# Kernel tuning notes

Measured on AMD Instinct MI355X. Metric: run time of the kernel, lower is better.

The kernel has to match this reference:

```python
import jax, jax.numpy as jnp
import numpy as np

B, T, E, H, R = 4, 256, 128, 8, 64
D = E // H


def _xavier(k, fan_in, fan_out, gain=1.0):
    a = gain * np.sqrt(6.0 / (fan_in + fan_out))
    return jax.random.uniform(k, (fan_in, fan_out), minval=-a, maxval=a, dtype=jnp.float32)


def setup_inputs() -> dict:
    key = jax.random.key(0)
    ks = jax.random.split(key, 16)
    g = 1.0 / np.sqrt(2.0)  # gain used for q/k/v when qkv_same_dim
    return {
        "query": jax.random.normal(ks[0], (B, T, E), jnp.float32),
        "velocity": jax.random.normal(ks[1], (B, T, 3, E), jnp.float32),
        "edge_feature": jax.random.normal(ks[2], (B, T, T, R), jnp.float32),
        "edge_direction": jax.random.normal(ks[3], (B, T, T, 3), jnp.float32),
        "cutoff": jax.random.uniform(ks[4], (B, T, T), jnp.float32),
        "Wq": _xavier(ks[5], E, E, g), "bq": jnp.zeros((E,), jnp.float32),
        "Wk": _xavier(ks[6], E, E, g), "bk": jnp.zeros((E,), jnp.float32),
        "Wv": _xavier(ks[7], E, 3 * E, g), "bv": jnp.zeros((3 * E,), jnp.float32),
        "Wo": _xavier(ks[8], E, 3 * E), "bo": jnp.zeros((3 * E,), jnp.float32),
        "Wvel": _xavier(ks[9], E, 3 * E), "bvel": jnp.zeros((3 * E,), jnp.float32),
        "Wdk": _xavier(ks[10], R, E), "bdk": jnp.zeros((E,), jnp.float32),
        "Wdv": _xavier(ks[11], R, 3 * E), "bdv": jnp.zeros((3 * E,), jnp.float32),
    }


def reference(query, velocity, edge_feature, edge_direction, cutoff,
              Wq, bq, Wk, bk, Wv, bv, Wo, bo, Wvel, bvel, Wdk, bdk, Wdv, bdv):
    b, t, e = query.shape
    h = H
    d = e // h
    scaling = d ** -0.5
    # projections
    q = ((query @ Wq + bq) * scaling).reshape(b, t, 1, h, d)   # [b,t,1,h,d]
    k = (query @ Wk + bk).reshape(b, 1, t, h, d)                # [b,1,t,h,d]
    v = (query @ Wv + bv).reshape(b, 1, t, h, 3 * d)            # [b,1,t,h,3d]
    # RBF distance gates (dense pairwise)
    dk = jax.nn.silu(edge_feature @ Wdk + bdk).reshape(b, t, t, h, d)
    dv = jax.nn.silu(edge_feature @ Wdv + bdv).reshape(b, t, t, h, 3 * d)
    v = v * dv                                                  # [b,t,t,h,3d]
    v, vp1, vp2 = jnp.split(v, 3, axis=-1)                      # each [b,t,t,h,d]
    # velocity channel
    velp = velocity @ Wvel + bvel                               # [b,t,3,3e]
    w1, w2, w3 = jnp.split(velp, 3, axis=-1)                    # each [b,t,3,e]
    velocity_dot = (w1 * w2).sum(axis=2)                        # [b,t,e]
    vel_r = velocity.reshape(b, t, 3, h, d)
    # elementwise (non-dot-product) attention weights
    aw = q * k * dk / np.float32(np.sqrt(d))                    # [b,t,t,h,d]
    awf = jnp.nan_to_num(jax.nn.softmax(aw, axis=2))
    c = cutoff[..., None, None]                                 # [b,t,t,1,1]
    attn = (awf * c * v * (c != 0)).sum(axis=2).reshape(b, t, e)
    o1, o2, o3 = jnp.split(attn @ Wo + bo, 3, axis=-1)          # each [b,t,e]
    # equivariant vector path
    vec1 = vel_r[:, None] * vp1[:, :, :, None]                  # [b,t,t,3,h,d]
    vec2 = vp2[:, :, :, None] * edge_direction[..., None, None]
    vec = ((vec1 + vec2).reshape(b, t, t, 3, e) * (c != 0)).sum(axis=2)  # [b,t,3,e]
    dx = velocity_dot * o2 + o3                                 # [b,t,e]
    dvec = w3 * o1[:, :, None, :] + vec                         # [b,t,3,e]
    return dx, dvec
```

## Files before the change

kernel.cpp:

```cpp
#include <hip/hip_runtime.h>
#include <hip/hip_bf16.h>
#include <math.h>

#define TT 256
#define EE 128
#define TJ 16

typedef __attribute__((ext_vector_type(8))) short short8v;
typedef __attribute__((ext_vector_type(4))) float f32x4;

__device__ __forceinline__ float silu_f(float x) {
    return x * __builtin_amdgcn_rcpf(1.0f + __expf(-x));
}

__device__ __forceinline__ unsigned short f2bf(float f) {
    union { float f; unsigned u; } x; x.f = f;
    unsigned r = (x.u + 0x7FFFu + ((x.u >> 16) & 1u)) >> 16;
    return (unsigned short)r;
}

__device__ __forceinline__ unsigned cvt_pk_bf16(float lo, float hi) {
    unsigned r;
    asm("v_cvt_pk_bf16_f32 %0, %1, %2" : "=v"(r) : "v"(lo), "v"(hi));
    return r;
}

__device__ __forceinline__ float bflo(unsigned u) { return __uint_as_float(u << 16); }
__device__ __forceinline__ float bfhi(unsigned u) { return __uint_as_float(u & 0xffff0000u); }

__global__ __launch_bounds__(256) void packW_kernel(
    const float* __restrict__ Wdk, const float* __restrict__ Wdv,
    unsigned short* __restrict__ wfrag) {
    const int idx = blockIdx.x * 256 + threadIdx.x;
    const int lane = idx & 63;
    const int kh = (idx >> 6) & 1;
    const int nn = (idx >> 7) & 7;
    const int w = idx >> 10;
    const float* Wsel; int wstride, colbase;
    if (w == 0) { Wsel = Wdk; wstride = 128; colbase = 0; }
    else { Wsel = Wdv; wstride = 384; colbase = (w - 1) * 128; }
    const int lrow = lane >> 4;
    const int lcol = lane & 15;
    const int col = colbase + nn * 16 + lcol;
    unsigned short* dst = wfrag + (size_t)idx * 8;
#pragma unroll
    for (int e = 0; e < 8; ++e) {
        const int k = kh * 32 + lrow * 8 + e;
        dst[e] = f2bf(Wsel[k * wstride + col]);
    }
}

__global__ __launch_bounds__(256) void phaseA_kernel(
    const float* __restrict__ query, const float* __restrict__ velocity,
    const float* __restrict__ Wq, const float* __restrict__ bq,
    const float* __restrict__ Wk, const float* __restrict__ bk,
    const float* __restrict__ Wv, const float* __restrict__ bv,
    const float* __restrict__ Wvel, const float* __restrict__ bvel,
    float* __restrict__ qs_ws, float* __restrict__ kk_ws,
    float* __restrict__ vproj_ws, float* __restrict__ veldot_ws,
    float* __restrict__ w3_ws) {
    const int row = blockIdx.x;
    const int t = threadIdx.x;
    __shared__ float sIn[EE];
    __shared__ float sVel[3 * EE];
    __shared__ float sVelp[3 * 384];
    if (t < EE) sIn[t] = query[(size_t)row * EE + t];
    for (int idx = t; idx < 3 * EE; idx += 256)
        sVel[idx] = velocity[(size_t)row * 3 * EE + idx];
    __syncthreads();

    for (int o = t; o < 640; o += 256) {
        if (o < 128) {
            int c = o;
            float acc = bq[c];
#pragma unroll 8
            for (int r = 0; r < 128; ++r) acc = fmaf(sIn[r], Wq[r * 128 + c], acc);
            qs_ws[(size_t)row * 128 + c] = acc * 0.25f;
        } else if (o < 256) {
            int c = o - 128;
            float acc = bk[c];
#pragma unroll 8
            for (int r = 0; r < 128; ++r) acc = fmaf(sIn[r], Wk[r * 128 + c], acc);
            kk_ws[(size_t)row * 128 + c] = acc;
        } else {
            int c = o - 256;
            float acc = bv[c];
#pragma unroll 8
            for (int r = 0; r < 128; ++r) acc = fmaf(sIn[r], Wv[r * 384 + c], acc);
            vproj_ws[(size_t)row * 384 + c] = acc;
        }
    }
    for (int c = t; c < 384; c += 256) {
        float a0 = bvel[c], a1 = a0, a2 = a0;
#pragma unroll 8
        for (int r = 0; r < 128; ++r) {
            float w = Wvel[r * 384 + c];
            a0 = fmaf(sVel[r], w, a0);
            a1 = fmaf(sVel[128 + r], w, a1);
            a2 = fmaf(sVel[256 + r], w, a2);
        }
        sVelp[0 * 384 + c] = a0;
        sVelp[1 * 384 + c] = a1;
        sVelp[2 * 384 + c] = a2;
    }
    __syncthreads();
    if (t < 128) {
        int c = t;
        float vd = 0.f;
#pragma unroll
        for (int s = 0; s < 3; ++s)
            vd += sVelp[s * 384 + c] * sVelp[s * 384 + 128 + c];
        veldot_ws[(size_t)row * 128 + c] = vd;
#pragma unroll
        for (int s = 0; s < 3; ++s)
            w3_ws[((size_t)row * 3 + s) * 128 + c] = sVelp[s * 384 + 256 + c];
    }
}

__global__ __launch_bounds__(256, 4) void phaseB_kernel(
    const float* __restrict__ edge_feature, const float* __restrict__ edge_direction,
    const float* __restrict__ cutoff, const float* __restrict__ velocity,
    const unsigned short* __restrict__ wfrag,
    const float* __restrict__ bdk, const float* __restrict__ bdv,
    const float* __restrict__ qs_ws, const float* __restrict__ kk_ws,
    const float* __restrict__ vproj_ws,
    float* __restrict__ attn_ws, float* __restrict__ vec_ws) {
    const int blk = blockIdx.x;
    const int x = blk & 7;
    const int slot = blk >> 3;
    const int b = x >> 1;
    const int i = ((x & 1) << 7) + slot;
    const int row = b * TT + i;

    const int t = threadIdx.x;
    const int wave = t >> 6;
    const int lane = t & 63;
    const int lrow = lane >> 4;
    const int lcol = lane & 15;

    __shared__ __align__(16) unsigned char sEFb[16 * 128];
    __shared__ unsigned short sKD[128 * 18];
    __shared__ unsigned short sGV[3 * 128 * 18];
    __shared__ float sCut[TJ];
    __shared__ float sDirS[TJ * 3];
    __shared__ float sMrg[128][5];

    const float* Bsel;
    int colbase;
    if (wave == 0) { Bsel = bdk; colbase = 0; }
    else { Bsel = bdv; colbase = (wave - 1) * 128; }

    float biasv[8];
#pragma unroll
    for (int n = 0; n < 8; ++n)
        biasv[n] = Bsel[colbase + n * 16 + lcol];

    const unsigned short* wfbase = wfrag + ((size_t)wave * 1024 + lane) * 8;

    const float* gsrc = (wave == 0) ? (kk_ws + (size_t)(b * TT) * 128)
                                    : (vproj_ws + (size_t)(b * TT) * 384);
    const int gstride = (wave == 0) ? 128 : 384;

    const int grp = t >> 7;
    const int c = t & 127;
    const float qsc = qs_ws[(size_t)row * 128 + c] * 0.25f;

    float l = 0.f, A = 0.f;
    float v0 = 0.f, v1 = 0.f, v2 = 0.f;

    const size_t ef_base = (size_t)row * TT * 64;
    const size_t cut_base = (size_t)row * TT;
    const size_t dir_base = (size_t)row * TT * 3;
    const float* velbase = velocity + (size_t)(b * TT) * 384 + c;

    f32x4 pEf = ((const f32x4*)(edge_feature + ef_base))[t];
    float pCut = (t < TJ) ? cutoff[cut_base + t] : 0.f;
    float pDir = (t < TJ * 3) ? edge_direction[dir_base + t] : 0.f;

    for (int j0 = 0; j0 < TT; j0 += TJ) {
        {
            const int erow = t >> 4;
            const int kq = t & 15;
            unsigned plo = cvt_pk_bf16(pEf[0], pEf[1]);
            unsigned phi = cvt_pk_bf16(pEf[2], pEf[3]);
            const int byteoff = (kq * 8) ^ ((erow & 7) << 4);
            *(int2*)(sEFb + erow * 128 + byteoff) = make_int2((int)plo, (int)phi);
            if (t < TJ) sCut[t] = pCut;
            if (t < TJ * 3) sDirS[t] = pDir;
        }
        __syncthreads();

        {
            const int arow = lcol;
            const int swzb = (arow & 7) << 4;
            const short8v a0 = *(const short8v*)(sEFb + arow * 128 + ((lrow * 16) ^ swzb));
            const short8v a1 = *(const short8v*)(sEFb + arow * 128 + ((64 + lrow * 16) ^ swzb));
            const int jb = j0 + lrow * 4;

            float gg[8][4];
#pragma unroll
            for (int n = 0; n < 8; ++n) {
                const float* gp = gsrc + (size_t)jb * gstride + colbase + n * 16 + lcol;
                gg[n][0] = gp[0];
                gg[n][1] = gp[gstride];
                gg[n][2] = gp[2 * gstride];
                gg[n][3] = gp[3 * gstride];
            }
#pragma unroll
            for (int n = 0; n < 8; ++n) {
                const int col = colbase + n * 16 + lcol;
                const short8v b0 = *(const short8v*)(wfbase + (size_t)n * 1024);
                const short8v b1 = *(const short8v*)(wfbase + (size_t)n * 1024 + 512);
                f32x4 acc = {biasv[n], biasv[n], biasv[n], biasv[n]};
                acc = __builtin_amdgcn_mfma_f32_16x16x32_bf16(a0, b0, acc, 0, 0, 0);
                acc = __builtin_amdgcn_mfma_f32_16x16x32_bf16(a1, b1, acc, 0, 0, 0);
                const float r0 = gg[n][0] * silu_f(acc[0]);
                const float r1 = gg[n][1] * silu_f(acc[1]);
                const float r2 = gg[n][2] * silu_f(acc[2]);
                const float r3 = gg[n][3] * silu_f(acc[3]);
                const unsigned w01 = cvt_pk_bf16(r0, r1);
                const unsigned w23 = cvt_pk_bf16(r2, r3);
                unsigned short* dst;
                if (wave == 0) {
                    dst = &sKD[col * 18 + lrow * 4];
                } else {
                    const int plane = (col >> 4) % 3;
                    const int cch = (col / 48) * 16 + lcol;
                    dst = &sGV[plane * 2304 + cch * 18 + lrow * 4];
                }
                *(unsigned*)(dst) = w01;
                *(unsigned*)(dst + 2) = w23;
            }
        }

        {
            const int jn = (j0 + TJ) & 255;
            pEf = ((const f32x4*)(edge_feature + ef_base + (size_t)jn * 64))[t];
            pCut = (t < TJ) ? cutoff[cut_base + jn + t] : 0.f;
            pDir = (t < TJ * 3) ? edge_direction[dir_base + (size_t)jn * 3 + t] : 0.f;
        }
        __syncthreads();

        {
            const int jlo = grp * (TJ / 2);
#pragma unroll
            for (int q = 0; q < 4; ++q) {
                const int jj = jlo + 2 * q;
                const unsigned kd2 = *(const unsigned*)(&sKD[c * 18 + jj]);
                const unsigned vg2 = *(const unsigned*)(&sGV[0 * 2304 + c * 18 + jj]);
                const unsigned p12 = *(const unsigned*)(&sGV[1 * 2304 + c * 18 + jj]);
                const unsigned p22 = *(const unsigned*)(&sGV[2 * 2304 + c * 18 + jj]);
                const float cut0 = sCut[jj];
                const float cut1 = sCut[jj + 1];
                const float p0 = __expf(qsc * bflo(kd2));
                const float p1 = __expf(qsc * bfhi(kd2));
                l += p0 + p1;
                A = fmaf(p0 * cut0, bflo(vg2), A);
                A = fmaf(p1 * cut1, bfhi(vg2), A);
                if (cut0 != 0.0f) {
                    const float* vp = velbase + (size_t)(j0 + jj) * 384;
                    const float w1 = bflo(p12), w2 = bflo(p22);
                    v0 = fmaf(vp[0],   w1, fmaf(w2, sDirS[jj * 3 + 0], v0));
                    v1 = fmaf(vp[128], w1, fmaf(w2, sDirS[jj * 3 + 1], v1));
                    v2 = fmaf(vp[256], w1, fmaf(w2, sDirS[jj * 3 + 2], v2));
                }
                if (cut1 != 0.0f) {
                    const float* vp = velbase + (size_t)(j0 + jj + 1) * 384;
                    const float w1 = bfhi(p12), w2 = bfhi(p22);
                    v0 = fmaf(vp[0],   w1, fmaf(w2, sDirS[jj * 3 + 3], v0));
                    v1 = fmaf(vp[128], w1, fmaf(w2, sDirS[jj * 3 + 4], v1));
                    v2 = fmaf(vp[256], w1, fmaf(w2, sDirS[jj * 3 + 5], v2));
                }
            }
        }
        __syncthreads();
    }

    if (grp == 1) {
        sMrg[c][0] = l;  sMrg[c][1] = A;
        sMrg[c][2] = v0; sMrg[c][3] = v1; sMrg[c][4] = v2;
    }
    __syncthreads();
    if (grp == 0) {
        const float L = l + sMrg[c][0];
        const float Aa = A + sMrg[c][1];
        const float attn = (L > 0.f) ? (Aa * __builtin_amdgcn_rcpf(L)) : 0.f;
        attn_ws[(size_t)row * 128 + c] = attn;
        vec_ws[((size_t)row * 3 + 0) * 128 + c] = v0 + sMrg[c][2];
        vec_ws[((size_t)row * 3 + 1) * 128 + c] = v1 + sMrg[c][3];
        vec_ws[((size_t)row * 3 + 2) * 128 + c] = v2 + sMrg[c][4];
    }
}

__global__ __launch_bounds__(256) void phaseC_kernel(
    const float* __restrict__ Wo, const float* __restrict__ bo,
    const float* __restrict__ attn_ws, const float* __restrict__ veldot_ws,
    const float* __restrict__ w3_ws, const float* __restrict__ vec_ws,
    float* __restrict__ out) {
    const int row = blockIdx.x;
    const int t = threadIdx.x;
    __shared__ float sAttn[128];
    __shared__ float sO[384];
    if (t < 128) sAttn[t] = attn_ws[(size_t)row * 128 + t];
    __syncthreads();
    for (int o = t; o < 384; o += 256) {
        float acc = bo[o];
#pragma unroll 8
        for (int r = 0; r < 128; ++r) acc = fmaf(sAttn[r], Wo[r * 384 + o], acc);
        sO[o] = acc;
    }
    __syncthreads();
    if (t < 128) {
        int c = t;
        float o1 = sO[c], o2 = sO[128 + c], o3 = sO[256 + c];
        float dx = fmaf(veldot_ws[(size_t)row * 128 + c], o2, o3);
        out[(size_t)row * 128 + c] = dx;
#pragma unroll
        for (int s = 0; s < 3; ++s) {
            size_t idx = ((size_t)row * 3 + s) * 128 + c;
            out[131072 + idx] = fmaf(w3_ws[idx], o1, vec_ws[idx]);
        }
    }
}

extern "C" void kernel_launch(void* const* d_in, const int* in_sizes, int n_in,
                              void* d_out, int out_size, void* d_ws, size_t ws_size,
                              hipStream_t stream) {
    (void)in_sizes; (void)n_in; (void)out_size; (void)ws_size;
    const float* query          = (const float*)d_in[0];
    const float* velocity       = (const float*)d_in[1];
    const float* edge_feature   = (const float*)d_in[2];
    const float* edge_direction = (const float*)d_in[3];
    const float* cutoff         = (const float*)d_in[4];
    const float* Wq   = (const float*)d_in[5];  const float* bq   = (const float*)d_in[6];
    const float* Wk   = (const float*)d_in[7];  const float* bk   = (const float*)d_in[8];
    const float* Wv   = (const float*)d_in[9];  const float* bv   = (const float*)d_in[10];
    const float* Wo   = (const float*)d_in[11]; const float* bo   = (const float*)d_in[12];
    const float* Wvel = (const float*)d_in[13]; const float* bvel = (const float*)d_in[14];
    const float* Wdk  = (const float*)d_in[15]; const float* bdk  = (const float*)d_in[16];
    const float* Wdv  = (const float*)d_in[17]; const float* bdv  = (const float*)d_in[18];

    float* ws        = (float*)d_ws;
    float* qs_ws     = ws;
    float* kk_ws     = ws + 131072;
    float* vproj_ws  = ws + 262144;
    float* veldot_ws = ws + 655360;
    float* w3_ws     = ws + 786432;
    float* attn_ws   = ws + 1179648;
    float* vec_ws    = ws + 1310720;
    unsigned short* wfrag = (unsigned short*)(ws + 1703936);

    float* out = (float*)d_out;

    hipLaunchKernelGGL(packW_kernel, dim3(16), dim3(256), 0, stream,
        Wdk, Wdv, wfrag);
    hipLaunchKernelGGL(phaseA_kernel, dim3(1024), dim3(256), 0, stream,
        query, velocity, Wq, bq, Wk, bk, Wv, bv, Wvel, bvel,
        qs_ws, kk_ws, vproj_ws, veldot_ws, w3_ws);
    hipLaunchKernelGGL(phaseB_kernel, dim3(1024), dim3(256), 0, stream,
        edge_feature, edge_direction, cutoff, velocity,
        wfrag, bdk, bdv, qs_ws, kk_ws, vproj_ws, attn_ws, vec_ws);
    hipLaunchKernelGGL(phaseC_kernel, dim3(1024), dim3(256), 0, stream,
        Wo, bo, attn_ws, veldot_ws, w3_ws, vec_ws, out);
}
```

Before: 186.9 us.

## Split phaseB attention over two key-column halves and merge partials in phaseC

The edge-attention kernel now launches twice as many blocks. Each block covers one query row and half of the key positions, and writes partial softmax denominators, numerators and vector sums to a workspace. The output kernel adds the two halves before the normalization divide and the vector output. This is meant to give the scheduler finer-grained work and a shorter per-block serial loop. In exchange it adds a second prefetch prologue per row, extra partial-result traffic and more reads in the final kernel.

```diff
diff --git a/kernel.cpp b/kernel.cpp
--- a/kernel.cpp
+++ b/kernel.cpp
@@ -5,6 +5,8 @@
 #define TT 256
 #define EE 128
 #define TJ 16
+#define NJH 2
+#define JSPAN 128
 
 typedef __attribute__((ext_vector_type(8))) short short8v;
 typedef __attribute__((ext_vector_type(4))) float f32x4;
@@ -124,12 +126,14 @@
     const float* __restrict__ bdk, const float* __restrict__ bdv,
     const float* __restrict__ qs_ws, const float* __restrict__ kk_ws,
     const float* __restrict__ vproj_ws,
-    float* __restrict__ attn_ws, float* __restrict__ vec_ws) {
+    float* __restrict__ part_ws) {
     const int blk = blockIdx.x;
-    const int x = blk & 7;
+    const int xcd = blk & 7;
     const int slot = blk >> 3;
-    const int b = x >> 1;
-    const int i = ((x & 1) << 7) + slot;
+    const int b = xcd >> 1;
+    const int jh = xcd & 1;
+    const int i = slot;
+    const int jbase = jh * JSPAN;
     const int row = b * TT + i;
 
     const int t = threadIdx.x;
@@ -173,11 +177,12 @@
     const size_t dir_base = (size_t)row * TT * 3;
     const float* velbase = velocity + (size_t)(b * TT) * 384 + c;
 
-    f32x4 pEf = ((const f32x4*)(edge_feature + ef_base))[t];
-    float pCut = (t < TJ) ? cutoff[cut_base + t] : 0.f;
-    float pDir = (t < TJ * 3) ? edge_direction[dir_base + t] : 0.f;
-
-    for (int j0 = 0; j0 < TT; j0 += TJ) {
+    f32x4 pEf = ((const f32x4*)(edge_feature + ef_base + (size_t)jbase * 64))[t];
+    float pCut = (t < TJ) ? cutoff[cut_base + jbase + t] : 0.f;
+    float pDir = (t < TJ * 3) ? edge_direction[dir_base + (size_t)jbase * 3 + t] : 0.f;
+
+    for (int jt = 0; jt < JSPAN; jt += TJ) {
+        const int j0 = jbase + jt;
         {
             const int erow = t >> 4;
             const int kq = t & 15;
@@ -234,7 +239,7 @@
         }
 
         {
-            const int jn = (j0 + TJ) & 255;
+            const int jn = jbase + ((jt + TJ) & (JSPAN - 1));
             pEf = ((const f32x4*)(edge_feature + ef_base + (size_t)jn * 64))[t];
             pCut = (t < TJ) ? cutoff[cut_base + jn + t] : 0.f;
             pDir = (t < TJ * 3) ? edge_direction[dir_base + (size_t)jn * 3 + t] : 0.f;
@@ -282,26 +287,31 @@
     }
     __syncthreads();
     if (grp == 0) {
-        const float L = l + sMrg[c][0];
-        const float Aa = A + sMrg[c][1];
-        const float attn = (L > 0.f) ? (Aa * __builtin_amdgcn_rcpf(L)) : 0.f;
-        attn_ws[(size_t)row * 128 + c] = attn;
-        vec_ws[((size_t)row * 3 + 0) * 128 + c] = v0 + sMrg[c][2];
-        vec_ws[((size_t)row * 3 + 1) * 128 + c] = v1 + sMrg[c][3];
-        vec_ws[((size_t)row * 3 + 2) * 128 + c] = v2 + sMrg[c][4];
+        float* P = part_ws + ((size_t)(row * NJH + jh) * 5) * 128 + c;
+        P[0 * 128] = l + sMrg[c][0];
+        P[1 * 128] = A + sMrg[c][1];
+        P[2 * 128] = v0 + sMrg[c][2];
+        P[3 * 128] = v1 + sMrg[c][3];
+        P[4 * 128] = v2 + sMrg[c][4];
     }
 }
 
 __global__ __launch_bounds__(256) void phaseC_kernel(
     const float* __restrict__ Wo, const float* __restrict__ bo,
-    const float* __restrict__ attn_ws, const float* __restrict__ veldot_ws,
-    const float* __restrict__ w3_ws, const float* __restrict__ vec_ws,
+    const float* __restrict__ part_ws, const float* __restrict__ veldot_ws,
+    const float* __restrict__ w3_ws,
     float* __restrict__ out) {
     const int row = blockIdx.x;
     const int t = threadIdx.x;
     __shared__ float sAttn[128];
     __shared__ float sO[384];
-    if (t < 128) sAttn[t] = attn_ws[(size_t)row * 128 + t];
+    const float* P0 = part_ws + ((size_t)(row * NJH + 0) * 5) * 128;
+    const float* P1 = part_ws + ((size_t)(row * NJH + 1) * 5) * 128;
+    if (t < 128) {
+        const float L = P0[0 * 128 + t] + P1[0 * 128 + t];
+        const float Aa = P0[1 * 128 + t] + P1[1 * 128 + t];
+        sAttn[t] = (L > 0.f) ? (Aa * __builtin_amdgcn_rcpf(L)) : 0.f;
+    }
     __syncthreads();
     for (int o = t; o < 384; o += 256) {
         float acc = bo[o];
@@ -318,7 +328,8 @@
 #pragma unroll
         for (int s = 0; s < 3; ++s) {
             size_t idx = ((size_t)row * 3 + s) * 128 + c;
-            out[131072 + idx] = fmaf(w3_ws[idx], o1, vec_ws[idx]);
+            const float vsum = P0[(2 + s) * 128 + c] + P1[(2 + s) * 128 + c];
+            out[131072 + idx] = fmaf(w3_ws[idx], o1, vsum);
         }
     }
 }
@@ -346,9 +357,8 @@
     float* vproj_ws  = ws + 262144;
     float* veldot_ws = ws + 655360;
     float* w3_ws     = ws + 786432;
-    float* attn_ws   = ws + 1179648;
-    float* vec_ws    = ws + 1310720;
-    unsigned short* wfrag = (unsigned short*)(ws + 1703936);
+    float* part_ws   = ws + 1179648;
+    unsigned short* wfrag = (unsigned short*)(ws + 2490368);
 
     float* out = (float*)d_out;
 
@@ -357,9 +367,9 @@
     hipLaunchKernelGGL(phaseA_kernel, dim3(1024), dim3(256), 0, stream,
         query, velocity, Wq, bq, Wk, bk, Wv, bv, Wvel, bvel,
         qs_ws, kk_ws, vproj_ws, veldot_ws, w3_ws);
-    hipLaunchKernelGGL(phaseB_kernel, dim3(1024), dim3(256), 0, stream,
+    hipLaunchKernelGGL(phaseB_kernel, dim3(2048), dim3(256), 0, stream,
         edge_feature, edge_direction, cutoff, velocity,
-        wfrag, bdk, bdv, qs_ws, kk_ws, vproj_ws, attn_ws, vec_ws);
+        wfrag, bdk, bdv, qs_ws, kk_ws, vproj_ws, part_ws);
     hipLaunchKernelGGL(phaseC_kernel, dim3(1024), dim3(256), 0, stream,
-        Wo, bo, attn_ws, veldot_ws, w3_ws, vec_ws, out);
-}
+        Wo, bo, part_ws, veldot_ws, w3_ws, out);
+}
```

Measured after the change: 191.6 us. +2.5%, slower.
